# Performance work log

Measured on AMD Instinct MI355X. Metric: run time of the kernel, lower is better.

## Reference

```python
import jax, jax.numpy as jnp
import numpy as np

D_MODEL = 1024
N_HEADS = 16
N_EXPERTS = 8
TOP_K = 2
EXPERT_HIDDEN = D_MODEL * 4 // N_EXPERTS  # 512, per MoELayer default


def layer_norm(x, g, b, eps=1e-5):
    mu = jnp.mean(x, axis=-1, keepdims=True)
    var = jnp.var(x, axis=-1, keepdims=True)
    return (x - mu) * jax.lax.rsqrt(var + eps) * g + b


def setup_inputs() -> dict:
    key = jax.random.key(0)
    ks = jax.random.split(key, 12)
    s = 1.0 / np.sqrt(D_MODEL)
    return {
        "x": jax.random.normal(ks[0], (2, 2048, D_MODEL), dtype=jnp.float32),
        "Wq": jax.random.normal(ks[1], (D_MODEL, D_MODEL), dtype=jnp.float32) * s,
        "Wk": jax.random.normal(ks[2], (D_MODEL, D_MODEL), dtype=jnp.float32) * s,
        "Wv": jax.random.normal(ks[3], (D_MODEL, D_MODEL), dtype=jnp.float32) * s,
        "Wo": jax.random.normal(ks[4], (D_MODEL, D_MODEL), dtype=jnp.float32) * s,
        "g1": jnp.ones((D_MODEL,), jnp.float32),
        "b1": jnp.zeros((D_MODEL,), jnp.float32),
        "g2": jnp.ones((D_MODEL,), jnp.float32),
        "b2": jnp.zeros((D_MODEL,), jnp.float32),
        "Wg": jax.random.normal(ks[5], (D_MODEL, N_EXPERTS), dtype=jnp.float32) * s,
        "W1": jax.random.normal(ks[6], (N_EXPERTS, D_MODEL, EXPERT_HIDDEN), dtype=jnp.float32) * s,
        "W2": jax.random.normal(ks[7], (N_EXPERTS, EXPERT_HIDDEN, D_MODEL), dtype=jnp.float32) * (1.0 / np.sqrt(EXPERT_HIDDEN)),
    }


def reference(x, Wq, Wk, Wv, Wo, g1, b1, g2, b2, Wg, W1, W2):
    B, S, D = x.shape
    H, dk = N_HEADS, D // N_HEADS

    # ---- pre-norm attention + residual (dropout = identity in eval) ----
    xn = layer_norm(x, g1, b1)
    q = (xn @ Wq).reshape(B, S, H, dk).transpose(0, 2, 1, 3)  # [B,H,S,dk]
    k = (xn @ Wk).reshape(B, S, H, dk).transpose(0, 2, 1, 3)
    v = (xn @ Wv).reshape(B, S, H, dk).transpose(0, 2, 1, 3)
    scores = jnp.einsum("bhqd,bhkd->bhqk", q, k) / np.sqrt(dk)
    attn = jax.nn.softmax(scores, axis=-1)
    o = jnp.einsum("bhqk,bhkd->bhqd", attn, v)
    o = o.transpose(0, 2, 1, 3).reshape(B, S, D) @ Wo
    x = x + o

    # ---- pre-norm MoE + residual ----
    xn2 = layer_norm(x, g2, b2)
    xf = xn2.reshape(B * S, D)  # [T, D]
    gate = xf @ Wg  # [T, E]
    topv, topi = jax.lax.top_k(gate, TOP_K)  # [T, K]
    probs = jax.nn.softmax(topv, axis=-1)    # softmax over top-k scores
    # dense combine weights [T, E] (top-k indices are distinct)
    cw = jnp.sum(jax.nn.one_hot(topi, N_EXPERTS, dtype=xf.dtype) * probs[..., None], axis=1)
    h = jax.nn.relu(jnp.einsum("td,edh->teh", xf, W1))  # [T,E,Hid]
    y = jnp.einsum("teh,ehd->ted", h, W2)               # [T,E,D]
    moe = jnp.einsum("ted,te->td", y, cw).reshape(B, S, D)
    return x + moe
```

## Files before the change

### kernel.cpp

```cpp
#include <hip/hip_runtime.h>

typedef __attribute__((ext_vector_type(8))) _Float16 f16x8;
typedef __attribute__((ext_vector_type(4))) _Float16 f16x4;
typedef __attribute__((ext_vector_type(2))) _Float16 f16x2;
typedef __attribute__((ext_vector_type(2))) __fp16 fp16x2_n;
typedef __attribute__((ext_vector_type(8))) short bf16x8;
typedef __attribute__((ext_vector_type(4))) float f32x4;
typedef __attribute__((ext_vector_type(4))) unsigned short u16x4;
typedef __attribute__((ext_vector_type(4))) float fx4;

#define D_MODEL 1024
#define N_HEADS 16
#define SEQ 2048
#define TOKENS 4096
#define N_EXP 8
#define EHID 512
#define LO_S 2048.0f
#define INV_LO (1.0f / 2048.0f)
#define QSCALE 0.18033688011112043f
#define DTHR 11.0f

__device__ inline unsigned short f2bf(float f) {
  union { float f; unsigned u; } v; v.f = f;
  unsigned u = v.u;
  return (unsigned short)((u + 0x7FFFu + ((u >> 16) & 1u)) >> 16);
}

__device__ inline void split16(float v, _Float16& h, _Float16& l) {
  h = (_Float16)v;
  l = (_Float16)((v - (float)h) * LO_S);
}

__device__ inline void split2(float a, float b, f16x2& h, f16x2& l) {
  fp16x2_n hn = __builtin_amdgcn_cvt_pkrtz(a, b);
  h = __builtin_bit_cast(f16x2, hn);
  fp16x2_n ln = __builtin_amdgcn_cvt_pkrtz((a - (float)h[0]) * LO_S, (b - (float)h[1]) * LO_S);
  l = __builtin_bit_cast(f16x2, ln);
}

__device__ inline void gload_lds16(const void* g, void* lds) {
  __builtin_amdgcn_global_load_lds((const __attribute__((address_space(1))) void*)g,
                                   (__attribute__((address_space(3))) void*)lds, 16, 0, 0);
}

__global__ __launch_bounds__(256) void prep_ln_kernel(const float* __restrict__ x, const float* __restrict__ g1,
                                                      const float* __restrict__ b1,
                                                      _Float16* __restrict__ xh, _Float16* __restrict__ xl,
                                                      const float* __restrict__ Wq, const float* __restrict__ Wk,
                                                      const float* __restrict__ Wv, const float* __restrict__ Wo,
                                                      const float* __restrict__ W1, const float* __restrict__ W2,
                                                      _Float16* __restrict__ qkvh, _Float16* __restrict__ qkvl,
                                                      _Float16* __restrict__ woh, _Float16* __restrict__ wol,
                                                      unsigned short* __restrict__ W1T, unsigned short* __restrict__ W2T,
                                                      int* __restrict__ cnt, int* __restrict__ perm) {
  int bb = blockIdx.x;
  if (bb < 4096) {
    int t = bb, tid = threadIdx.x;
    const float* row = x + (size_t)t * D_MODEL;
    fx4 v = *(const fx4*)(row + tid * 4);
    float s = v[0] + v[1] + v[2] + v[3];
    float s2 = v[0]*v[0] + v[1]*v[1] + v[2]*v[2] + v[3]*v[3];
    #pragma unroll
    for (int off = 1; off < 64; off <<= 1) { s += __shfl_xor(s, off); s2 += __shfl_xor(s2, off); }
    __shared__ float red[8];
    int wv = tid >> 6, wl = tid & 63;
    if (wl == 0) { red[wv] = s; red[4 + wv] = s2; }
    __syncthreads();
    s = red[0] + red[1] + red[2] + red[3];
    s2 = red[4] + red[5] + red[6] + red[7];
    float mu = s * (1.f / 1024.f);
    float var = s2 * (1.f / 1024.f) - mu * mu;
    float rstd = rsqrtf(var + 1e-5f);
    int kk = tid * 4;
    f16x4 oh, ol;
    #pragma unroll
    for (int c = 0; c < 4; c++) {
      float y = (v[c] - mu) * rstd * g1[kk + c] + b1[kk + c];
      _Float16 h, lo; split16(y, h, lo);
      oh[c] = h; ol[c] = lo;
    }
    *(f16x4*)(xh + (size_t)t * D_MODEL + kk) = oh;
    *(f16x4*)(xl + (size_t)t * D_MODEL + kk) = ol;
    return;
  }
  int b = bb - 4096;
  if (b >= 12288) {
    int i = (b - 12288) * 256 + threadIdx.x;
    if (i < 8) cnt[i] = 0;
    if (i < 8704) perm[i] = 0;
    return;
  }
  __shared__ float tile[32][33];
  int tx = threadIdx.x & 31, ty = threadIdx.x >> 5;
  if (b < 4096) {
    int z = b >> 10, rem = b & 1023;
    int c0 = (rem & 31) * 32, r0 = (rem >> 5) * 32;
    const float* src = (z == 0) ? Wq : (z == 1) ? Wk : (z == 2) ? Wv : Wo;
    _Float16* dh = (z < 3) ? qkvh + (size_t)z * 1048576 : woh;
    _Float16* dl = (z < 3) ? qkvl + (size_t)z * 1048576 : wol;
    #pragma unroll
    for (int i = 0; i < 4; i++) tile[ty + 8*i][tx] = src[(size_t)(r0 + ty + 8*i) * 1024 + c0 + tx];
    __syncthreads();
    #pragma unroll
    for (int i = 0; i < 4; i++) {
      float v = tile[tx][ty + 8*i];
      _Float16 h, lo; split16(v, h, lo);
      size_t idx = (size_t)(c0 + ty + 8*i) * 1024 + r0 + tx;
      dh[idx] = h; dl[idx] = lo;
    }
  } else if (b < 8192) {
    int q = b - 4096, z = q >> 9, rem = q & 511;
    int c0 = (rem & 15) * 32, r0 = (rem >> 4) * 32;
    const float* src = W1 + (size_t)z * 524288;
    unsigned short* dst = W1T + (size_t)z * 524288;
    #pragma unroll
    for (int i = 0; i < 4; i++) tile[ty + 8*i][tx] = src[(size_t)(r0 + ty + 8*i) * 512 + c0 + tx];
    __syncthreads();
    #pragma unroll
    for (int i = 0; i < 4; i++) dst[(size_t)(c0 + ty + 8*i) * 1024 + r0 + tx] = f2bf(tile[tx][ty + 8*i]);
  } else {
    int q = b - 8192, z = q >> 9, rem = q & 511;
    int c0 = (rem & 31) * 32, r0 = (rem >> 5) * 32;
    const float* src = W2 + (size_t)z * 524288;
    unsigned short* dst = W2T + (size_t)z * 524288;
    #pragma unroll
    for (int i = 0; i < 4; i++) tile[ty + 8*i][tx] = src[(size_t)(r0 + ty + 8*i) * 1024 + c0 + tx];
    __syncthreads();
    #pragma unroll
    for (int i = 0; i < 4; i++) dst[(size_t)(c0 + ty + 8*i) * 512 + r0 + tx] = f2bf(tile[tx][ty + 8*i]);
  }
}

__device__ inline void gemm128s(const _Float16* __restrict__ Ah, const _Float16* __restrict__ Al,
                                const _Float16* __restrict__ Bh, const _Float16* __restrict__ Bl,
                                int lda, int ldb, int K, int bm, int bn,
                                _Float16* lsbuf, f32x4 (&acc)[4][4], f32x4 (&accx)[4][4]) {
  const int tid = threadIdx.x, w = tid >> 6, l = tid & 63, lr = l & 15, lg = l >> 4;
  const int wr = (w >> 1) * 64, wc = (w & 1) * 64;
  int ca = (((tid & 3) ^ ((tid >> 3) & 3)) * 8);
  int ra0 = tid >> 2, ra1 = 64 + (tid >> 2);
  const _Float16* gA0 = Ah + (size_t)(bm + ra0) * lda + ca;
  const _Float16* gA1 = Ah + (size_t)(bm + ra1) * lda + ca;
  const _Float16* gA2 = Al + (size_t)(bm + ra0) * lda + ca;
  const _Float16* gA3 = Al + (size_t)(bm + ra1) * lda + ca;
  const _Float16* gB0 = Bh + (size_t)(bn + ra0) * ldb + ca;
  const _Float16* gB1 = Bh + (size_t)(bn + ra1) * ldb + ca;
  const _Float16* gB2 = Bl + (size_t)(bn + ra0) * ldb + ca;
  const _Float16* gB3 = Bl + (size_t)(bn + ra1) * ldb + ca;
  char* base = (char*)lsbuf;
  const int wo = w * 1024;
#define STAGE8(bb_, ko) do { \
    gload_lds16(gA0 + (ko), (bb_) + wo);         gload_lds16(gA1 + (ko), (bb_) + 4096 + wo);  \
    gload_lds16(gA2 + (ko), (bb_) + 8192 + wo);  gload_lds16(gA3 + (ko), (bb_) + 12288 + wo); \
    gload_lds16(gB0 + (ko), (bb_) + 16384 + wo); gload_lds16(gB1 + (ko), (bb_) + 20480 + wo); \
    gload_lds16(gB2 + (ko), (bb_) + 24576 + wo); gload_lds16(gB3 + (ko), (bb_) + 28672 + wo); } while (0)
  STAGE8(base, 0);
  __syncthreads();
  const int swzB = ((lg ^ ((lr >> 1) & 3)) << 4);
  int cur = 0;
  for (int ko = 0; ko < K; ko += 32) {
    char* bR = base + cur * 32768;
    if (ko + 32 < K) STAGE8(base + (cur ^ 1) * 32768, ko + 32);
    f16x8 ah[4], al4[4], bh4[4], bl4[4];
    #pragma unroll
    for (int m = 0; m < 4; m++) {
      int roff = (wr + m * 16 + lr) * 64 + swzB;
      ah[m]  = *(const f16x8*)(bR + roff);
      al4[m] = *(const f16x8*)(bR + 8192 + roff);
    }
    #pragma unroll
    for (int n = 0; n < 4; n++) {
      int roff = (wc + n * 16 + lr) * 64 + swzB;
      bh4[n] = *(const f16x8*)(bR + 16384 + roff);
      bl4[n] = *(const f16x8*)(bR + 24576 + roff);
    }
    __builtin_amdgcn_s_setprio(1);
    #pragma unroll
    for (int m = 0; m < 4; m++)
      #pragma unroll
      for (int n = 0; n < 4; n++) {
        acc[m][n]  = __builtin_amdgcn_mfma_f32_16x16x32_f16(ah[m], bh4[n], acc[m][n], 0, 0, 0);
        accx[m][n] = __builtin_amdgcn_mfma_f32_16x16x32_f16(ah[m], bl4[n], accx[m][n], 0, 0, 0);
        accx[m][n] = __builtin_amdgcn_mfma_f32_16x16x32_f16(al4[m], bh4[n], accx[m][n], 0, 0, 0);
      }
    __builtin_amdgcn_s_setprio(0);
    __syncthreads();
    cur ^= 1;
  }
#undef STAGE8
}

__global__ __launch_bounds__(256) void gemm_qkv_kernel(const _Float16* __restrict__ xh, const _Float16* __restrict__ xl,
                                                       const _Float16* __restrict__ Wh, const _Float16* __restrict__ Wl,
                                                       _Float16* __restrict__ qh, _Float16* __restrict__ ql,
                                                       _Float16* __restrict__ kh, _Float16* __restrict__ kl,
                                                       _Float16* __restrict__ vh, _Float16* __restrict__ vl) {
  __shared__ _Float16 ls[32768];
  f32x4 acc[4][4] = {}, accx[4][4] = {};
  int bid = blockIdx.x;
  int sw = (bid & 7) * 96 + (bid >> 3);
  int bm = (sw & 31) * 128, bn = (sw >> 5) * 128;
  gemm128s(xh, xl, Wh, Wl, 1024, 1024, 1024, bm, bn, ls, acc, accx);
  const int tid = threadIdx.x, w = tid >> 6, l = tid & 63, lr = l & 15, lg = l >> 4;
  const int wr = (w >> 1) * 64, wc = (w & 1) * 64;
  #pragma unroll
  for (int m = 0; m < 4; m++) {
    int row0 = bm + wr + m * 16 + lg * 4;
    #pragma unroll
    for (int n = 0; n < 4; n++) {
      int col = bn + wc + n * 16 + lr;
      int mat = col >> 10;
      int c = col & 1023, h = c >> 6, d = c & 63;
      if (mat == 2) {
        int bb = row0 >> 11, ss = row0 & 2047;
        int tile = ss >> 5, kvs = ss & 31;
        f16x4 ph, pl;
        #pragma unroll
        for (int j = 0; j < 4; j++) {
          float v = acc[m][n][j] + accx[m][n][j] * INV_LO;
          _Float16 hh, ll; split16(v, hh, ll);
          ph[j] = hh; pl[j] = ll;
        }
        size_t base = ((size_t)(bb * N_HEADS + h) * 64 + tile) * 2048;
        int off = d * 32 + ((((kvs >> 3) ^ ((d >> 1) & 3)) << 3) | (kvs & 7));
        *(f16x4*)(vh + base + off) = ph;
        *(f16x4*)(vl + base + off) = pl;
      } else if (mat == 1) {
        #pragma unroll
        for (int j = 0; j < 4; j++) {
          float v = acc[m][n][j] + accx[m][n][j] * INV_LO;
          _Float16 hh, ll; split16(v, hh, ll);
          int t = row0 + j, bb = t >> 11, ss = t & 2047;
          int tile = ss >> 5, r = ss & 31;
          size_t base = ((size_t)(bb * N_HEADS + h) * 64 + tile) * 2048;
          int off = r * 64 + ((((d >> 3) ^ (r & 7)) << 3) | (d & 7));
          kh[base + off] = hh; kl[base + off] = ll;
        }
      } else {
        #pragma unroll
        for (int j = 0; j < 4; j++) {
          float v = (acc[m][n][j] + accx[m][n][j] * INV_LO) * QSCALE;
          _Float16 hh, ll; split16(v, hh, ll);
          int t = row0 + j, bb = t >> 11, ss = t & 2047;
          size_t idx = ((size_t)(bb * N_HEADS + h) * SEQ + ss) * 64 + d;
          qh[idx] = hh; ql[idx] = ll;
        }
      }
    }
  }
}

__global__ __launch_bounds__(256, 4) void flash_kernel(const _Float16* __restrict__ qhp, const _Float16* __restrict__ qlp,
                                                       const _Float16* __restrict__ khs, const _Float16* __restrict__ kls,
                                                       const _Float16* __restrict__ vhs, const _Float16* __restrict__ vls,
                                                       _Float16* __restrict__ oh, _Float16* __restrict__ ol) {
  __shared__ _Float16 lsKV[2][8192];
  __shared__ _Float16 lsP[4][2][512];
  int wgid = blockIdx.x;
  int xcd = wgid & 7, kk = wgid >> 3;
  int bh = xcd * 4 + (kk >> 5), qt = kk & 31;
  int tid = threadIdx.x, w = tid >> 6, l = tid & 63, lr = l & 15, lg = l >> 4;
  int q0 = qt * 64 + w * 16;
  const _Float16* qhb = qhp + (size_t)bh * SEQ * 64;
  const _Float16* qlb = qlp + (size_t)bh * SEQ * 64;
  f16x8 qfh[2], qfl[2];
  #pragma unroll
  for (int ks = 0; ks < 2; ks++) {
    size_t idx = (size_t)(q0 + lr) * 64 + ks * 32 + lg * 8;
    qfh[ks] = *(const f16x8*)(qhb + idx);
    qfl[ks] = *(const f16x8*)(qlb + idx);
  }
  const _Float16* splane = (w == 0) ? khs : (w == 1) ? kls : (w == 2) ? vhs : vls;
  const _Float16* sbase = splane + (size_t)bh * 131072 + l * 8;

  f32x4 acc[4] = {}, accx[4] = {};
  float mst = -1e30f, lstp = 0.f;

  {
    const _Float16* sp = sbase;
    _Float16* dd = &lsKV[0][w * 2048];
    gload_lds16(sp, dd); gload_lds16(sp + 512, dd + 512);
    gload_lds16(sp + 1024, dd + 1024); gload_lds16(sp + 1536, dd + 1536);
  }
  __syncthreads();

  for (int t = 0; t < 64; t++) {
    int bR = t & 1;
    if (t < 63) {
      const _Float16* sp = sbase + (size_t)(t + 1) * 2048;
      _Float16* dd = &lsKV[bR ^ 1][w * 2048];
      gload_lds16(sp, dd); gload_lds16(sp + 512, dd + 512);
      gload_lds16(sp + 1024, dd + 1024); gload_lds16(sp + 1536, dd + 1536);
    }
    char* bufB = (char*)&lsKV[bR][0];

    f32x4 s[2] = {}, sx[2] = {};
    #pragma unroll
    for (int ks = 0; ks < 2; ks++) {
      f16x8 kfh[2], kfl[2];
      #pragma unroll
      for (int m = 0; m < 2; m++) {
        int off = (m * 16 + lr) * 128 + (((ks * 4 + lg) ^ (lr & 7)) << 4);
        kfh[m] = *(const f16x8*)(bufB + off);
        kfl[m] = *(const f16x8*)(bufB + 4096 + off);
      }
      __builtin_amdgcn_s_setprio(1);
      #pragma unroll
      for (int m = 0; m < 2; m++) {
        s[m]  = __builtin_amdgcn_mfma_f32_16x16x32_f16(kfh[m], qfh[ks], s[m], 0, 0, 0);
        sx[m] = __builtin_amdgcn_mfma_f32_16x16x32_f16(kfh[m], qfl[ks], sx[m], 0, 0, 0);
        sx[m] = __builtin_amdgcn_mfma_f32_16x16x32_f16(kfl[m], qfh[ks], sx[m], 0, 0, 0);
      }
      __builtin_amdgcn_s_setprio(0);
    }

    float tm = -3e38f;
    #pragma unroll
    for (int m = 0; m < 2; m++)
      #pragma unroll
      for (int j = 0; j < 4; j++) {
        s[m][j] += sx[m][j] * INV_LO;
        tm = fmaxf(tm, s[m][j]);
      }
    if (!__all(tm - mst <= DTHR)) {
      tm = fmaxf(tm, __shfl_xor(tm, 16));
      tm = fmaxf(tm, __shfl_xor(tm, 32));
      float mnew = fmaxf(mst, tm);
      float corr = exp2f(mst - mnew);
      #pragma unroll
      for (int m2 = 0; m2 < 4; m2++)
        #pragma unroll
        for (int j = 0; j < 4; j++) { acc[m2][j] *= corr; accx[m2][j] *= corr; }
      lstp *= corr;
      mst = mnew;
    }
    #pragma unroll
    for (int m = 0; m < 2; m++) {
      #pragma unroll
      for (int j = 0; j < 4; j++) {
        float p = exp2f(s[m][j] - mst);
        lstp += p;
        s[m][j] = p;
      }
      f16x2 h01, h23, l01, l23;
      split2(s[m][0], s[m][1], h01, l01);
      split2(s[m][2], s[m][3], h23, l23);
      f16x4 ph, pl;
      ph[0] = h01[0]; ph[1] = h01[1]; ph[2] = h23[0]; ph[3] = h23[1];
      pl[0] = l01[0]; pl[1] = l01[1]; pl[2] = l23[0]; pl[3] = l23[1];
      int boff = lr * 64 + ((((m * 2 + (lg >> 1)) ^ ((lr >> 1) & 3)) << 4) | ((lg & 1) * 8));
      *(f16x4*)((char*)&lsP[w][0][0] + boff) = ph;
      *(f16x4*)((char*)&lsP[w][1][0] + boff) = pl;
    }

    int poff = lr * 64 + ((lg ^ ((lr >> 1) & 3)) << 4);
    f16x8 pfh = *(const f16x8*)((char*)&lsP[w][0][0] + poff);
    f16x8 pfl = *(const f16x8*)((char*)&lsP[w][1][0] + poff);
    __builtin_amdgcn_s_setprio(1);
    #pragma unroll
    for (int m2 = 0; m2 < 4; m2++) {
      int voff = (m2 * 16 + lr) * 64 + ((lg ^ ((lr >> 1) & 3)) << 4);
      f16x8 vfh = *(const f16x8*)(bufB + 8192 + voff);
      f16x8 vfl = *(const f16x8*)(bufB + 12288 + voff);
      acc[m2]  = __builtin_amdgcn_mfma_f32_16x16x32_f16(vfh, pfh, acc[m2], 0, 0, 0);
      accx[m2] = __builtin_amdgcn_mfma_f32_16x16x32_f16(vfh, pfl, accx[m2], 0, 0, 0);
      accx[m2] = __builtin_amdgcn_mfma_f32_16x16x32_f16(vfl, pfh, accx[m2], 0, 0, 0);
    }
    __builtin_amdgcn_s_setprio(0);
    __syncthreads();
  }

  float lst = lstp + __shfl_xor(lstp, 16);
  lst += __shfl_xor(lst, 32);
  float inv = 1.f / lst;
  int b = bh >> 4, h = bh & 15;
  int tkn = b * SEQ + q0 + lr;
  #pragma unroll
  for (int m2 = 0; m2 < 4; m2++) {
    f16x4 ph, pl;
    #pragma unroll
    for (int j = 0; j < 4; j++) {
      float o = (acc[m2][j] + accx[m2][j] * INV_LO) * inv;
      _Float16 hh, ll; split16(o, hh, ll);
      ph[j] = hh; pl[j] = ll;
    }
    size_t idx = (size_t)tkn * D_MODEL + h * 64 + m2 * 16 + lg * 4;
    *(f16x4*)(oh + idx) = ph;
    *(f16x4*)(ol + idx) = pl;
  }
}

__global__ __launch_bounds__(256) void gemm_oproj_kernel(const _Float16* __restrict__ ah, const _Float16* __restrict__ al,
                                                         const _Float16* __restrict__ Wh, const _Float16* __restrict__ Wl,
                                                         const float* __restrict__ x, float* __restrict__ out) {
  __shared__ _Float16 ls[32768];
  f32x4 acc[4][4] = {}, accx[4][4] = {};
  int bid = blockIdx.x;
  int sw = (bid & 7) * 32 + (bid >> 3);
  int bm = (sw & 31) * 128, bn = (sw >> 5) * 128;
  gemm128s(ah, al, Wh, Wl, 1024, 1024, 1024, bm, bn, ls, acc, accx);
  const int tid = threadIdx.x, w = tid >> 6, l = tid & 63, lr = l & 15, lg = l >> 4;
  const int wr = (w >> 1) * 64, wc = (w & 1) * 64;
  #pragma unroll
  for (int m = 0; m < 4; m++) {
    int row0 = bm + wr + m * 16 + lg * 4;
    #pragma unroll
    for (int n = 0; n < 4; n++) {
      int col = bn + wc + n * 16 + lr;
      #pragma unroll
      for (int j = 0; j < 4; j++) {
        size_t idx = (size_t)(row0 + j) * D_MODEL + col;
        out[idx] = (acc[m][n][j] + accx[m][n][j] * INV_LO) + x[idx];
      }
    }
  }
}

__global__ __launch_bounds__(256) void gate_kernel(const float* __restrict__ x1, const float* __restrict__ Wg,
                                                   const float* __restrict__ g2, const float* __restrict__ b2,
                                                   unsigned short* __restrict__ xn2,
                                                   int* __restrict__ cnt, int* __restrict__ topi,
                                                   float* __restrict__ topw) {
  int t = blockIdx.x * 4 + (threadIdx.x >> 6);
  int l = threadIdx.x & 63;
  const float* row = x1 + (size_t)t * D_MODEL;
  fx4 v[4];
  float s = 0.f, s2 = 0.f;
  #pragma unroll
  for (int i = 0; i < 4; i++) {
    v[i] = *(const fx4*)(row + l * 16 + i * 4);
    #pragma unroll
    for (int c = 0; c < 4; c++) { s += v[i][c]; s2 += v[i][c] * v[i][c]; }
  }
  #pragma unroll
  for (int off = 1; off < 64; off <<= 1) { s += __shfl_xor(s, off); s2 += __shfl_xor(s2, off); }
  float mu = s * (1.f / 1024.f);
  float var = s2 * (1.f / 1024.f) - mu * mu;
  float rstd = rsqrtf(var + 1e-5f);
  float a8[8] = {0,0,0,0,0,0,0,0};
  #pragma unroll
  for (int i = 0; i < 4; i++) {
    u16x4 ox;
    #pragma unroll
    for (int c = 0; c < 4; c++) {
      int kk = l * 16 + i * 4 + c;
      float xv = (v[i][c] - mu) * rstd * g2[kk] + b2[kk];
      ox[c] = f2bf(xv);
      const float* wr_ = Wg + (size_t)kk * 8;
      fx4 wa = *(const fx4*)wr_;
      fx4 wb = *(const fx4*)(wr_ + 4);
      a8[0] += xv * wa[0]; a8[1] += xv * wa[1]; a8[2] += xv * wa[2]; a8[3] += xv * wa[3];
      a8[4] += xv * wb[0]; a8[5] += xv * wb[1]; a8[6] += xv * wb[2]; a8[7] += xv * wb[3];
    }
    *(u16x4*)(xn2 + (size_t)t * D_MODEL + l * 16 + i * 4) = ox;
  }
  #pragma unroll
  for (int e = 0; e < 8; e++)
    #pragma unroll
    for (int off = 1; off < 64; off <<= 1) a8[e] += __shfl_xor(a8[e], off);
  if (l == 0) {
    int i0 = 0; float v0 = a8[0];
    #pragma unroll
    for (int e = 1; e < 8; e++) if (a8[e] > v0) { v0 = a8[e]; i0 = e; }
    int i1 = -1; float v1 = -3.4e38f;
    #pragma unroll
    for (int e = 0; e < 8; e++) if (e != i0 && a8[e] > v1) { v1 = a8[e]; i1 = e; }
    float p0 = 1.f / (1.f + __expf(v1 - v0));
    topi[t * 2] = i0; topi[t * 2 + 1] = i1;
    topw[t * 2] = p0; topw[t * 2 + 1] = 1.f - p0;
    atomicAdd(&cnt[i0], 1); atomicAdd(&cnt[i1], 1);
  }
}

__global__ __launch_bounds__(256) void scatter_kernel(const int* __restrict__ topi, const int* __restrict__ cnt,
                                                      int* __restrict__ perm, int* __restrict__ slot_of) {
  int e = blockIdx.x, tid = threadIdx.x;
  __shared__ int basesh;
  __shared__ int wsum[4];
  if (tid == 0) {
    int a = 0;
    for (int i = 0; i < e; i++) a += ((cnt[i] + 63) >> 6) << 6;
    basesh = a;
  }
  __syncthreads();
  for (int seg = 0; seg < 8192; seg += 256) {
    int a = seg + tid;
    int match = (topi[a] == e) ? 1 : 0;
    unsigned long long bal = __ballot(match);
    int wl = tid & 63, wv = tid >> 6;
    int lanepre = __popcll(bal & ((1ULL << wl) - 1ULL));
    if (wl == 0) wsum[wv] = __popcll(bal);
    __syncthreads();
    int wpre = 0;
    for (int i = 0; i < wv; i++) wpre += wsum[i];
    int total = wsum[0] + wsum[1] + wsum[2] + wsum[3];
    if (match) {
      int pos = basesh + wpre + lanepre;
      perm[pos] = a >> 1;
      slot_of[a] = pos;
    }
    __syncthreads();
    if (tid == 0) basesh += total;
    __syncthreads();
  }
}

__global__ __launch_bounds__(512) void moe_ffn_kernel(const unsigned short* __restrict__ xn2,
                                                      const unsigned short* __restrict__ W1T,
                                                      const unsigned short* __restrict__ W2T,
                                                      const int* __restrict__ cnt,
                                                      const int* __restrict__ perm,
                                                      float* __restrict__ y) {
  int bid = blockIdx.x;
  int e = -1, lt = bid, off = 0;
  for (int i = 0; i < 8; i++) {
    int nt = (cnt[i] + 63) >> 6;
    if (lt < nt) { e = i; break; }
    lt -= nt; off += nt << 6;
  }
  if (e < 0) return;
  int slot0 = off + lt * 64;

  __shared__ int t_sh[64];
  __shared__ unsigned short lsX[64 * 128];
  __shared__ unsigned short hsh[64 * 264];
  int tid = threadIdx.x, w = tid >> 6, l = tid & 63, lr = l & 15, lg = l >> 4;
  if (tid < 64) t_sh[tid] = perm[slot0 + tid];
  __syncthreads();

  const unsigned short* W1e = W1T + (size_t)e * EHID * D_MODEL;
  const unsigned short* W2e = W2T + (size_t)e * D_MODEL * EHID;

  f32x4 acc2[4][8] = {};
  for (int h = 0; h < 2; h++) {
    f32x4 acc1[4][2] = {};
    for (int kc = 0; kc < 8; kc++) {
      __syncthreads();
      #pragma unroll
      for (int L = 0; L < 2; L++) {
        int u = tid + 512 * L;
        int r = u >> 4, sp = u & 15;
        int cs = (sp & 8) | ((sp & 7) ^ (r & 7));
        gload_lds16(xn2 + (size_t)t_sh[r] * D_MODEL + kc * 128 + cs * 8, (char*)lsX + u * 16);
      }
      __syncthreads();
      #pragma unroll
      for (int kst = 0; kst < 4; kst++) {
        bf16x8 a[4];
        #pragma unroll
        for (int m = 0; m < 4; m++) {
          int row = m * 16 + lr;
          int slot = kst * 4 + lg;
          int cs = (slot & 8) | ((slot & 7) ^ (row & 7));
          a[m] = *(const bf16x8*)((char*)lsX + row * 256 + cs * 16);
        }
        int ko = kc * 128 + kst * 32;
        #pragma unroll
        for (int n = 0; n < 2; n++) {
          bf16x8 bb = *(const bf16x8*)(W1e + (size_t)(h * 256 + w * 32 + n * 16 + lr) * D_MODEL + ko + lg * 8);
          #pragma unroll
          for (int m = 0; m < 4; m++)
            acc1[m][n] = __builtin_amdgcn_mfma_f32_16x16x32_bf16(a[m], bb, acc1[m][n], 0, 0, 0);
        }
      }
    }
    __syncthreads();
    #pragma unroll
    for (int m = 0; m < 4; m++)
      #pragma unroll
      for (int n = 0; n < 2; n++)
        #pragma unroll
        for (int j = 0; j < 4; j++)
          hsh[(m*16 + lg*4 + j) * 264 + w * 32 + n * 16 + lr] = f2bf(fmaxf(acc1[m][n][j], 0.f));
    __syncthreads();
    for (int k2 = 0; k2 < 256; k2 += 32) {
      bf16x8 a2[4];
      #pragma unroll
      for (int m = 0; m < 4; m++) a2[m] = *(const bf16x8*)(hsh + (m*16 + lr) * 264 + k2 + lg * 8);
      #pragma unroll
      for (int n = 0; n < 8; n++) {
        bf16x8 bb = *(const bf16x8*)(W2e + (size_t)(w * 128 + n * 16 + lr) * EHID + h * 256 + k2 + lg * 8);
        #pragma unroll
        for (int m = 0; m < 4; m++)
          acc2[m][n] = __builtin_amdgcn_mfma_f32_16x16x32_bf16(a2[m], bb, acc2[m][n], 0, 0, 0);
      }
    }
  }
  #pragma unroll
  for (int m = 0; m < 4; m++)
    #pragma unroll
    for (int j = 0; j < 4; j++) {
      int r = m * 16 + lg * 4 + j;
      #pragma unroll
      for (int n = 0; n < 8; n++)
        y[(size_t)(slot0 + r) * D_MODEL + w * 128 + n * 16 + lr] = acc2[m][n][j];
    }
}

__global__ __launch_bounds__(256) void combine_kernel(const float* __restrict__ y, const int* __restrict__ slot_of,
                                                      const float* __restrict__ topw, float* __restrict__ out) {
  int t = blockIdx.x * 4 + (threadIdx.x >> 6);
  int l = threadIdx.x & 63;
  int s0 = slot_of[t * 2], s1 = slot_of[t * 2 + 1];
  float w0 = topw[t * 2], w1 = topw[t * 2 + 1];
  const float* y0 = y + (size_t)s0 * D_MODEL + l * 16;
  const float* y1 = y + (size_t)s1 * D_MODEL + l * 16;
  float* o = out + (size_t)t * D_MODEL + l * 16;
  #pragma unroll
  for (int i = 0; i < 4; i++) {
    fx4 av = *(const fx4*)(y0 + i * 4);
    fx4 bv = *(const fx4*)(y1 + i * 4);
    fx4 d = *(const fx4*)(o + i * 4);
    #pragma unroll
    for (int j = 0; j < 4; j++) d[j] += w0 * av[j] + w1 * bv[j];
    *(fx4*)(o + i * 4) = d;
  }
}

#define MB (1u << 20)
extern "C" void kernel_launch(void* const* d_in, const int* in_sizes, int n_in,
                              void* d_out, int out_size, void* d_ws, size_t ws_size,
                              hipStream_t stream) {
  const float* x  = (const float*)d_in[0];
  const float* Wq = (const float*)d_in[1];
  const float* Wk = (const float*)d_in[2];
  const float* Wv = (const float*)d_in[3];
  const float* Wo = (const float*)d_in[4];
  const float* g1 = (const float*)d_in[5];
  const float* b1 = (const float*)d_in[6];
  const float* g2 = (const float*)d_in[7];
  const float* b2 = (const float*)d_in[8];
  const float* Wg = (const float*)d_in[9];
  const float* W1 = (const float*)d_in[10];
  const float* W2 = (const float*)d_in[11];
  float* out = (float*)d_out;

  char* ws = (char*)d_ws;
  _Float16* xn1h = (_Float16*)(ws + 0*MB);
  _Float16* xn1l = (_Float16*)(ws + 8*MB);
  _Float16* Wqkh = (_Float16*)(ws + 16*MB);
  _Float16* Wqkl = (_Float16*)(ws + 22*MB);
  _Float16* Woh  = (_Float16*)(ws + 28*MB);
  _Float16* Wol  = (_Float16*)(ws + 30*MB);
  _Float16* qhb  = (_Float16*)(ws + 32*MB);
  _Float16* qlb  = (_Float16*)(ws + 40*MB);
  _Float16* khb  = (_Float16*)(ws + 48*MB);
  _Float16* klb  = (_Float16*)(ws + 56*MB);
  _Float16* vhb  = (_Float16*)(ws + 64*MB);
  _Float16* vlb  = (_Float16*)(ws + 72*MB);
  unsigned short* xn2 = (unsigned short*)(ws + 80*MB);
  unsigned short* W1T = (unsigned short*)(ws + 88*MB);
  unsigned short* W2T = (unsigned short*)(ws + 96*MB);
  char* misc = ws + 104*MB;
  int*   topi    = (int*)(misc);
  float* topw    = (float*)(misc + 32768);
  int*   slot_of = (int*)(misc + 65536);
  int*   cnt     = (int*)(misc + 98304);
  int*   perm    = (int*)(misc + 98368);
  float* ybuf    = (float*)(ws + 32*MB);
  _Float16* attnh = xn1h;
  _Float16* attnl = xn1l;

  prep_ln_kernel<<<16419, 256, 0, stream>>>(x, g1, b1, xn1h, xn1l,
                                            Wq, Wk, Wv, Wo, W1, W2,
                                            Wqkh, Wqkl, Woh, Wol, W1T, W2T, cnt, perm);

  gemm_qkv_kernel<<<768, 256, 0, stream>>>(xn1h, xn1l, Wqkh, Wqkl, qhb, qlb, khb, klb, vhb, vlb);
  flash_kernel<<<1024, 256, 0, stream>>>(qhb, qlb, khb, klb, vhb, vlb, attnh, attnl);
  gemm_oproj_kernel<<<256, 256, 0, stream>>>(attnh, attnl, Woh, Wol, x, out);

  gate_kernel<<<1024, 256, 0, stream>>>(out, Wg, g2, b2, xn2, cnt, topi, topw);
  scatter_kernel<<<8, 256, 0, stream>>>(topi, cnt, perm, slot_of);
  moe_ffn_kernel<<<136, 512, 0, stream>>>(xn2, W1T, W2T, cnt, perm, ybuf);
  combine_kernel<<<1024, 256, 0, stream>>>(ybuf, slot_of, topw, out);

  (void)in_sizes; (void)n_in; (void)out_size; (void)ws_size;
}
```

Baseline: 528.1 us.

## Double flash query tile per warp and restructure MoE FFN into small expert chunks

The flash attention kernel now gives each warp 32 query rows instead of 16, so every K/V tile staged in LDS is reused across twice as many queries. The grid is halved to 512 blocks and the occupancy hint drops to 2 blocks per CU to make room for the larger accumulator set. The MoE FFN kernel is rewritten to handle 32-token chunks per expert over a fixed 1024-block grid, computing the full 512-wide hidden layer in one pass and then the output in two halves. This raises parallelism for that kernel but reads expert weights from global memory more often, and the higher register use in flash may lower occupancy.

```diff
diff --git a/kernel.cpp b/kernel.cpp
--- a/kernel.cpp
+++ b/kernel.cpp
@@ -250,31 +250,34 @@
   }
 }
 
-__global__ __launch_bounds__(256, 4) void flash_kernel(const _Float16* __restrict__ qhp, const _Float16* __restrict__ qlp,
+__global__ __launch_bounds__(256, 2) void flash_kernel(const _Float16* __restrict__ qhp, const _Float16* __restrict__ qlp,
                                                        const _Float16* __restrict__ khs, const _Float16* __restrict__ kls,
                                                        const _Float16* __restrict__ vhs, const _Float16* __restrict__ vls,
                                                        _Float16* __restrict__ oh, _Float16* __restrict__ ol) {
   __shared__ _Float16 lsKV[2][8192];
-  __shared__ _Float16 lsP[4][2][512];
+  __shared__ _Float16 lsP[4][2][1024];
   int wgid = blockIdx.x;
   int xcd = wgid & 7, kk = wgid >> 3;
-  int bh = xcd * 4 + (kk >> 5), qt = kk & 31;
+  int bh = xcd * 4 + (kk >> 4), qt = kk & 15;
   int tid = threadIdx.x, w = tid >> 6, l = tid & 63, lr = l & 15, lg = l >> 4;
-  int q0 = qt * 64 + w * 16;
+  int q0 = qt * 128 + w * 32;
   const _Float16* qhb = qhp + (size_t)bh * SEQ * 64;
   const _Float16* qlb = qlp + (size_t)bh * SEQ * 64;
-  f16x8 qfh[2], qfl[2];
-  #pragma unroll
-  for (int ks = 0; ks < 2; ks++) {
-    size_t idx = (size_t)(q0 + lr) * 64 + ks * 32 + lg * 8;
-    qfh[ks] = *(const f16x8*)(qhb + idx);
-    qfl[ks] = *(const f16x8*)(qlb + idx);
-  }
+  f16x8 qfh[2][2], qfl[2][2];
+  #pragma unroll
+  for (int nf = 0; nf < 2; nf++)
+    #pragma unroll
+    for (int ks = 0; ks < 2; ks++) {
+      size_t idx = (size_t)(q0 + nf * 16 + lr) * 64 + ks * 32 + lg * 8;
+      qfh[nf][ks] = *(const f16x8*)(qhb + idx);
+      qfl[nf][ks] = *(const f16x8*)(qlb + idx);
+    }
   const _Float16* splane = (w == 0) ? khs : (w == 1) ? kls : (w == 2) ? vhs : vls;
   const _Float16* sbase = splane + (size_t)bh * 131072 + l * 8;
 
-  f32x4 acc[4] = {}, accx[4] = {};
-  float mst = -1e30f, lstp = 0.f;
+  f32x4 acc[4][2] = {}, accx[4][2] = {};
+  float mst = -1e30f;
+  float lstp[2] = {0.f, 0.f};
 
   {
     const _Float16* sp = sbase;
@@ -294,7 +297,7 @@
     }
     char* bufB = (char*)&lsKV[bR][0];
 
-    f32x4 s[2] = {}, sx[2] = {};
+    f32x4 s[2][2] = {}, sx[2][2] = {};
     #pragma unroll
     for (int ks = 0; ks < 2; ks++) {
       f16x8 kfh[2], kfl[2];
@@ -306,11 +309,13 @@
       }
       __builtin_amdgcn_s_setprio(1);
       #pragma unroll
-      for (int m = 0; m < 2; m++) {
-        s[m]  = __builtin_amdgcn_mfma_f32_16x16x32_f16(kfh[m], qfh[ks], s[m], 0, 0, 0);
-        sx[m] = __builtin_amdgcn_mfma_f32_16x16x32_f16(kfh[m], qfl[ks], sx[m], 0, 0, 0);
-        sx[m] = __builtin_amdgcn_mfma_f32_16x16x32_f16(kfl[m], qfh[ks], sx[m], 0, 0, 0);
-      }
+      for (int m = 0; m < 2; m++)
+        #pragma unroll
+        for (int nf = 0; nf < 2; nf++) {
+          s[m][nf]  = __builtin_amdgcn_mfma_f32_16x16x32_f16(kfh[m], qfh[nf][ks], s[m][nf], 0, 0, 0);
+          sx[m][nf] = __builtin_amdgcn_mfma_f32_16x16x32_f16(kfh[m], qfl[nf][ks], sx[m][nf], 0, 0, 0);
+          sx[m][nf] = __builtin_amdgcn_mfma_f32_16x16x32_f16(kfl[m], qfh[nf][ks], sx[m][nf], 0, 0, 0);
+        }
       __builtin_amdgcn_s_setprio(0);
     }
 
@@ -318,10 +323,12 @@
     #pragma unroll
     for (int m = 0; m < 2; m++)
       #pragma unroll
-      for (int j = 0; j < 4; j++) {
-        s[m][j] += sx[m][j] * INV_LO;
-        tm = fmaxf(tm, s[m][j]);
-      }
+      for (int nf = 0; nf < 2; nf++)
+        #pragma unroll
+        for (int j = 0; j < 4; j++) {
+          s[m][nf][j] += sx[m][nf][j] * INV_LO;
+          tm = fmaxf(tm, s[m][nf][j]);
+        }
     if (!__all(tm - mst <= DTHR)) {
       tm = fmaxf(tm, __shfl_xor(tm, 16));
       tm = fmaxf(tm, __shfl_xor(tm, 32));
@@ -330,63 +337,82 @@
       #pragma unroll
       for (int m2 = 0; m2 < 4; m2++)
         #pragma unroll
-        for (int j = 0; j < 4; j++) { acc[m2][j] *= corr; accx[m2][j] *= corr; }
-      lstp *= corr;
+        for (int nf = 0; nf < 2; nf++)
+          #pragma unroll
+          for (int j = 0; j < 4; j++) { acc[m2][nf][j] *= corr; accx[m2][nf][j] *= corr; }
+      lstp[0] *= corr; lstp[1] *= corr;
       mst = mnew;
     }
     #pragma unroll
-    for (int m = 0; m < 2; m++) {
-      #pragma unroll
-      for (int j = 0; j < 4; j++) {
-        float p = exp2f(s[m][j] - mst);
-        lstp += p;
-        s[m][j] = p;
-      }
-      f16x2 h01, h23, l01, l23;
-      split2(s[m][0], s[m][1], h01, l01);
-      split2(s[m][2], s[m][3], h23, l23);
-      f16x4 ph, pl;
-      ph[0] = h01[0]; ph[1] = h01[1]; ph[2] = h23[0]; ph[3] = h23[1];
-      pl[0] = l01[0]; pl[1] = l01[1]; pl[2] = l23[0]; pl[3] = l23[1];
-      int boff = lr * 64 + ((((m * 2 + (lg >> 1)) ^ ((lr >> 1) & 3)) << 4) | ((lg & 1) * 8));
-      *(f16x4*)((char*)&lsP[w][0][0] + boff) = ph;
-      *(f16x4*)((char*)&lsP[w][1][0] + boff) = pl;
-    }
-
-    int poff = lr * 64 + ((lg ^ ((lr >> 1) & 3)) << 4);
-    f16x8 pfh = *(const f16x8*)((char*)&lsP[w][0][0] + poff);
-    f16x8 pfl = *(const f16x8*)((char*)&lsP[w][1][0] + poff);
+    for (int nf = 0; nf < 2; nf++) {
+      int prow = nf * 16 + lr;
+      int pf = (prow >> 1) & 3;
+      #pragma unroll
+      for (int m = 0; m < 2; m++) {
+        #pragma unroll
+        for (int j = 0; j < 4; j++) {
+          float p = exp2f(s[m][nf][j] - mst);
+          lstp[nf] += p;
+          s[m][nf][j] = p;
+        }
+        f16x2 h01, h23, l01, l23;
+        split2(s[m][nf][0], s[m][nf][1], h01, l01);
+        split2(s[m][nf][2], s[m][nf][3], h23, l23);
+        f16x4 ph, pl;
+        ph[0] = h01[0]; ph[1] = h01[1]; ph[2] = h23[0]; ph[3] = h23[1];
+        pl[0] = l01[0]; pl[1] = l01[1]; pl[2] = l23[0]; pl[3] = l23[1];
+        int boff = prow * 64 + ((((2 * m + (lg >> 1)) ^ pf) << 4) | ((lg & 1) * 8));
+        *(f16x4*)((char*)&lsP[w][0][0] + boff) = ph;
+        *(f16x4*)((char*)&lsP[w][1][0] + boff) = pl;
+      }
+    }
+
+    f16x8 pfh[2], pfl[2];
+    #pragma unroll
+    for (int nf = 0; nf < 2; nf++) {
+      int prow = nf * 16 + lr;
+      int poff = prow * 64 + ((lg ^ ((prow >> 1) & 3)) << 4);
+      pfh[nf] = *(const f16x8*)((char*)&lsP[w][0][0] + poff);
+      pfl[nf] = *(const f16x8*)((char*)&lsP[w][1][0] + poff);
+    }
     __builtin_amdgcn_s_setprio(1);
     #pragma unroll
     for (int m2 = 0; m2 < 4; m2++) {
-      int voff = (m2 * 16 + lr) * 64 + ((lg ^ ((lr >> 1) & 3)) << 4);
+      int vrow = m2 * 16 + lr;
+      int voff = vrow * 64 + ((lg ^ ((vrow >> 1) & 3)) << 4);
       f16x8 vfh = *(const f16x8*)(bufB + 8192 + voff);
       f16x8 vfl = *(const f16x8*)(bufB + 12288 + voff);
-      acc[m2]  = __builtin_amdgcn_mfma_f32_16x16x32_f16(vfh, pfh, acc[m2], 0, 0, 0);
-      accx[m2] = __builtin_amdgcn_mfma_f32_16x16x32_f16(vfh, pfl, accx[m2], 0, 0, 0);
-      accx[m2] = __builtin_amdgcn_mfma_f32_16x16x32_f16(vfl, pfh, accx[m2], 0, 0, 0);
+      #pragma unroll
+      for (int nf = 0; nf < 2; nf++) {
+        acc[m2][nf]  = __builtin_amdgcn_mfma_f32_16x16x32_f16(vfh, pfh[nf], acc[m2][nf], 0, 0, 0);
+        accx[m2][nf] = __builtin_amdgcn_mfma_f32_16x16x32_f16(vfh, pfl[nf], accx[m2][nf], 0, 0, 0);
+        accx[m2][nf] = __builtin_amdgcn_mfma_f32_16x16x32_f16(vfl, pfh[nf], accx[m2][nf], 0, 0, 0);
+      }
     }
     __builtin_amdgcn_s_setprio(0);
     __syncthreads();
   }
 
-  float lst = lstp + __shfl_xor(lstp, 16);
-  lst += __shfl_xor(lst, 32);
-  float inv = 1.f / lst;
   int b = bh >> 4, h = bh & 15;
-  int tkn = b * SEQ + q0 + lr;
-  #pragma unroll
-  for (int m2 = 0; m2 < 4; m2++) {
-    f16x4 ph, pl;
-    #pragma unroll
-    for (int j = 0; j < 4; j++) {
-      float o = (acc[m2][j] + accx[m2][j] * INV_LO) * inv;
-      _Float16 hh, ll; split16(o, hh, ll);
-      ph[j] = hh; pl[j] = ll;
-    }
-    size_t idx = (size_t)tkn * D_MODEL + h * 64 + m2 * 16 + lg * 4;
-    *(f16x4*)(oh + idx) = ph;
-    *(f16x4*)(ol + idx) = pl;
+  #pragma unroll
+  for (int nf = 0; nf < 2; nf++) {
+    float lst = lstp[nf] + __shfl_xor(lstp[nf], 16);
+    lst += __shfl_xor(lst, 32);
+    float inv = 1.f / lst;
+    int tkn = b * SEQ + q0 + nf * 16 + lr;
+    #pragma unroll
+    for (int m2 = 0; m2 < 4; m2++) {
+      f16x4 ph, pl;
+      #pragma unroll
+      for (int j = 0; j < 4; j++) {
+        float o = (acc[m2][nf][j] + accx[m2][nf][j] * INV_LO) * inv;
+        _Float16 hh, ll; split16(o, hh, ll);
+        ph[j] = hh; pl[j] = ll;
+      }
+      size_t idx = (size_t)tkn * D_MODEL + h * 64 + m2 * 16 + lg * 4;
+      *(f16x4*)(oh + idx) = ph;
+      *(f16x4*)(ol + idx) = pl;
+    }
   }
 }
 
@@ -505,96 +531,83 @@
   }
 }
 
-__global__ __launch_bounds__(512) void moe_ffn_kernel(const unsigned short* __restrict__ xn2,
+__global__ __launch_bounds__(256) void moe_ffn_kernel(const unsigned short* __restrict__ xn2,
                                                       const unsigned short* __restrict__ W1T,
                                                       const unsigned short* __restrict__ W2T,
                                                       const int* __restrict__ cnt,
                                                       const int* __restrict__ perm,
                                                       float* __restrict__ y) {
-  int bid = blockIdx.x;
-  int e = -1, lt = bid, off = 0;
-  for (int i = 0; i < 8; i++) {
-    int nt = (cnt[i] + 63) >> 6;
-    if (lt < nt) { e = i; break; }
-    lt -= nt; off += nt << 6;
-  }
-  if (e < 0) return;
-  int slot0 = off + lt * 64;
-
-  __shared__ int t_sh[64];
-  __shared__ unsigned short lsX[64 * 128];
-  __shared__ unsigned short hsh[64 * 264];
+  int e = blockIdx.x & 7, chunk = blockIdx.x >> 3;
+  if (chunk * 32 >= cnt[e]) return;
+  int base = 0;
+  #pragma unroll
+  for (int i = 0; i < 8; i++) if (i < e) base += ((cnt[i] + 63) >> 6) << 6;
+  int slot0 = base + chunk * 32;
+
+  __shared__ int t_sh[32];
+  __shared__ unsigned short lsX[32 * 32];
+  __shared__ unsigned short hsh[32 * 520];
   int tid = threadIdx.x, w = tid >> 6, l = tid & 63, lr = l & 15, lg = l >> 4;
-  if (tid < 64) t_sh[tid] = perm[slot0 + tid];
+  if (tid < 32) t_sh[tid] = perm[slot0 + tid];
   __syncthreads();
 
+  int Xr = tid >> 2;
+  int Xc = (((tid & 3) ^ ((tid >> 3) & 3)) * 8);
+  const unsigned short* gX = xn2 + (size_t)(tid < 128 ? t_sh[Xr & 31] : 0) * D_MODEL + Xc;
   const unsigned short* W1e = W1T + (size_t)e * EHID * D_MODEL;
   const unsigned short* W2e = W2T + (size_t)e * D_MODEL * EHID;
-
-  f32x4 acc2[4][8] = {};
-  for (int h = 0; h < 2; h++) {
-    f32x4 acc1[4][2] = {};
-    for (int kc = 0; kc < 8; kc++) {
-      __syncthreads();
-      #pragma unroll
-      for (int L = 0; L < 2; L++) {
-        int u = tid + 512 * L;
-        int r = u >> 4, sp = u & 15;
-        int cs = (sp & 8) | ((sp & 7) ^ (r & 7));
-        gload_lds16(xn2 + (size_t)t_sh[r] * D_MODEL + kc * 128 + cs * 8, (char*)lsX + u * 16);
-      }
-      __syncthreads();
-      #pragma unroll
-      for (int kst = 0; kst < 4; kst++) {
-        bf16x8 a[4];
-        #pragma unroll
-        for (int m = 0; m < 4; m++) {
-          int row = m * 16 + lr;
-          int slot = kst * 4 + lg;
-          int cs = (slot & 8) | ((slot & 7) ^ (row & 7));
-          a[m] = *(const bf16x8*)((char*)lsX + row * 256 + cs * 16);
-        }
-        int ko = kc * 128 + kst * 32;
-        #pragma unroll
-        for (int n = 0; n < 2; n++) {
-          bf16x8 bb = *(const bf16x8*)(W1e + (size_t)(h * 256 + w * 32 + n * 16 + lr) * D_MODEL + ko + lg * 8);
-          #pragma unroll
-          for (int m = 0; m < 4; m++)
-            acc1[m][n] = __builtin_amdgcn_mfma_f32_16x16x32_bf16(a[m], bb, acc1[m][n], 0, 0, 0);
-        }
-      }
-    }
-    __syncthreads();
-    #pragma unroll
-    for (int m = 0; m < 4; m++)
-      #pragma unroll
-      for (int n = 0; n < 2; n++)
-        #pragma unroll
-        for (int j = 0; j < 4; j++)
-          hsh[(m*16 + lg*4 + j) * 264 + w * 32 + n * 16 + lr] = f2bf(fmaxf(acc1[m][n][j], 0.f));
-    __syncthreads();
-    for (int k2 = 0; k2 < 256; k2 += 32) {
-      bf16x8 a2[4];
-      #pragma unroll
-      for (int m = 0; m < 4; m++) a2[m] = *(const bf16x8*)(hsh + (m*16 + lr) * 264 + k2 + lg * 8);
+  const int swz = ((lg ^ ((lr >> 1) & 3)) << 3);
+
+  f32x4 acc[2][8] = {};
+  for (int ko = 0; ko < D_MODEL; ko += 32) {
+    if (tid < 128) gload_lds16(gX + ko, (char*)lsX + w * 1024);
+    __syncthreads();
+    bf16x8 a[2];
+    #pragma unroll
+    for (int m = 0; m < 2; m++) a[m] = *(const bf16x8*)(lsX + (m*16 + lr) * 32 + swz);
+    #pragma unroll
+    for (int n = 0; n < 8; n++) {
+      bf16x8 bb = *(const bf16x8*)(W1e + (size_t)(w * 128 + n * 16 + lr) * D_MODEL + ko + lg * 8);
+      #pragma unroll
+      for (int m = 0; m < 2; m++)
+        acc[m][n] = __builtin_amdgcn_mfma_f32_16x16x32_bf16(a[m], bb, acc[m][n], 0, 0, 0);
+    }
+    __syncthreads();
+  }
+  #pragma unroll
+  for (int m = 0; m < 2; m++)
+    #pragma unroll
+    for (int n = 0; n < 8; n++)
+      #pragma unroll
+      for (int j = 0; j < 4; j++)
+        hsh[(m*16 + lg*4 + j) * 520 + w * 128 + n * 16 + lr] = f2bf(fmaxf(acc[m][n][j], 0.f));
+  __syncthreads();
+
+  for (int p = 0; p < 2; p++) {
+    f32x4 acc2[2][8] = {};
+    for (int k2 = 0; k2 < EHID; k2 += 32) {
+      bf16x8 a2[2];
+      #pragma unroll
+      for (int m = 0; m < 2; m++) a2[m] = *(const bf16x8*)(hsh + (m*16 + lr) * 520 + k2 + lg * 8);
       #pragma unroll
       for (int n = 0; n < 8; n++) {
-        bf16x8 bb = *(const bf16x8*)(W2e + (size_t)(w * 128 + n * 16 + lr) * EHID + h * 256 + k2 + lg * 8);
-        #pragma unroll
-        for (int m = 0; m < 4; m++)
+        int ycol = w * 256 + p * 128 + n * 16 + lr;
+        bf16x8 bb = *(const bf16x8*)(W2e + (size_t)ycol * EHID + k2 + lg * 8);
+        #pragma unroll
+        for (int m = 0; m < 2; m++)
           acc2[m][n] = __builtin_amdgcn_mfma_f32_16x16x32_bf16(a2[m], bb, acc2[m][n], 0, 0, 0);
       }
     }
-  }
-  #pragma unroll
-  for (int m = 0; m < 4; m++)
-    #pragma unroll
-    for (int j = 0; j < 4; j++) {
-      int r = m * 16 + lg * 4 + j;
-      #pragma unroll
-      for (int n = 0; n < 8; n++)
-        y[(size_t)(slot0 + r) * D_MODEL + w * 128 + n * 16 + lr] = acc2[m][n][j];
-    }
+    #pragma unroll
+    for (int m = 0; m < 2; m++)
+      #pragma unroll
+      for (int j = 0; j < 4; j++) {
+        int r = m * 16 + lg * 4 + j;
+        #pragma unroll
+        for (int n = 0; n < 8; n++)
+          y[(size_t)(slot0 + r) * D_MODEL + w * 256 + p * 128 + n * 16 + lr] = acc2[m][n][j];
+      }
+  }
 }
 
 __global__ __launch_bounds__(256) void combine_kernel(const float* __restrict__ y, const int* __restrict__ slot_of,
@@ -666,12 +679,12 @@
                                             Wqkh, Wqkl, Woh, Wol, W1T, W2T, cnt, perm);
 
   gemm_qkv_kernel<<<768, 256, 0, stream>>>(xn1h, xn1l, Wqkh, Wqkl, qhb, qlb, khb, klb, vhb, vlb);
-  flash_kernel<<<1024, 256, 0, stream>>>(qhb, qlb, khb, klb, vhb, vlb, attnh, attnl);
+  flash_kernel<<<512, 256, 0, stream>>>(qhb, qlb, khb, klb, vhb, vlb, attnh, attnl);
   gemm_oproj_kernel<<<256, 256, 0, stream>>>(attnh, attnl, Woh, Wol, x, out);
 
   gate_kernel<<<1024, 256, 0, stream>>>(out, Wg, g2, b2, xn2, cnt, topi, topw);
   scatter_kernel<<<8, 256, 0, stream>>>(topi, cnt, perm, slot_of);
-  moe_ffn_kernel<<<136, 512, 0, stream>>>(xn2, W1T, W2T, cnt, perm, ybuf);
+  moe_ffn_kernel<<<1024, 256, 0, stream>>>(xn2, W1T, W2T, cnt, perm, ybuf);
   combine_kernel<<<1024, 256, 0, stream>>>(ybuf, slot_of, topw, out);
 
   (void)in_sizes; (void)n_in; (void)out_size; (void)ws_size;
```

Result: slower. 572.1 us (+8.3%).
